# Optimization experiments

Hardware: AMD Instinct MI355X
Metric: run time of the kernel (lower is better)

## Reference

```python
import jax, jax.numpy as jnp
import numpy as np
from functools import partial

CHANNEL_N = 16
FIRE_RATE = 0.5
SCALE_GROWTH = 1.0
SCALE_GROWTH_SYNTH = 1.0
ANGLE = 0.0


def _sobel_kernels(angle, channel_n):
    # dx = outer([1,2,1],[-1,0,1])/8 ; dy = dx.T ; rotated by angle (degrees)
    dx = np.outer([1.0, 2.0, 1.0], [-1.0, 0.0, 1.0]) / 8.0
    dy = dx.T
    c, s = np.cos(angle * np.pi / 180.0), np.sin(angle * np.pi / 180.0)
    w1 = (c * dx - s * dy).astype(np.float32)
    w2 = (s * dx + c * dy).astype(np.float32)
    # depthwise conv weights, OIHW with O=channel_n, I=1 (groups=channel_n)
    k1 = jnp.asarray(np.tile(w1[None, None], (channel_n, 1, 1, 1)))
    k2 = jnp.asarray(np.tile(w2[None, None], (channel_n, 1, 1, 1)))
    return k1, k2


def _depthwise(x_nchw, k):
    return jax.lax.conv_general_dilated(
        x_nchw, k, window_strides=(1, 1), padding=((1, 1), (1, 1)),
        dimension_numbers=('NCHW', 'OIHW', 'NCHW'),
        feature_group_count=x_nchw.shape[1])


def _alive(x_nchw):
    # 3x3 max-pool (stride 1, pad 1) on channel 1, threshold 0.1
    a = x_nchw[:, 1:2]
    m = jax.lax.reduce_window(a, -jnp.inf, jax.lax.max,
                              (1, 1, 3, 3), (1, 1, 1, 1),
                              ((0, 0), (0, 0), (1, 1), (1, 1)))
    return m > 0.1


def _update(x, w0, b0, w1, key):
    # x: [B,H,W,C]; torch does x.transpose(1,3) -> [B,C,W,H]
    xt = jnp.transpose(x, (0, 3, 2, 1))
    pre_life = _alive(xt)
    k1, k2 = _sobel_kernels(ANGLE, xt.shape[1])
    y = jnp.concatenate([xt, _depthwise(xt, k1), _depthwise(xt, k2)], axis=1)  # [B,3C,W,H]
    d = jnp.transpose(y, (0, 3, 2, 1))  # [B,H,W,3C]
    h = jax.nn.relu(jnp.einsum('bhwc,cd->bhwd', d, w0) + b0)
    dx = jnp.einsum('bhwd,dc->bhwc', h, w1)
    stoch = (jax.random.uniform(key, dx.shape[:3] + (1,)) > FIRE_RATE).astype(dx.dtype)
    dx = dx * stoch * (SCALE_GROWTH * SCALE_GROWTH_SYNTH)
    xt = xt + jnp.transpose(dx, (0, 3, 2, 1))
    post_life = _alive(xt)
    xt = xt * (pre_life & post_life).astype(xt.dtype)
    return jnp.transpose(xt, (0, 3, 2, 1))


def setup_inputs() -> dict:
    key = jax.random.key(0)
    k1, k2, k3, k4 = jax.random.split(key, 4)
    B, H, W, C, HID = 16, 256, 256, CHANNEL_N, 128
    x = jax.random.uniform(k1, (B, H, W, C), dtype=jnp.float32)
    w0 = jax.random.normal(k2, (3 * C, HID), dtype=jnp.float32) * 0.05
    b0 = jax.random.normal(k3, (HID,), dtype=jnp.float32) * 0.05
    w1 = jax.random.normal(k4, (HID, C), dtype=jnp.float32) * 0.05
    return {'x': x, 'w0': w0, 'b0': b0, 'w1': w1, 'steps': 1}


def reference(x, w0, b0, w1, steps):
    key = jax.random.key(42)
    for step in range(steps):
        x = _update(x, w0, b0, w1, jax.random.fold_in(key, step))
    return x
```

## Files before the change

### kernel.cpp

```cpp
#include <hip/hip_runtime.h>
#include <hip/hip_bf16.h>

#define BB 16
#define HH 256
#define WW 256
#define CC 16
#define HID 128
#define NPIX (BB*HH*WW)
#define NBLK2 2048

#define PCL_STRIDE 36
#define PCL_WAVE2  (128*PCL_STRIDE)

typedef __attribute__((ext_vector_type(8))) short s16x8;
typedef __attribute__((ext_vector_type(4))) float f32x4;

union V8 { uint4 u; uint2 h[2]; s16x8 s; };

struct Key2 { unsigned a, b; };

__host__ __device__ constexpr unsigned rotl32c(unsigned x, int d) {
    return (x << d) | (x >> (32 - d));
}

__host__ __device__ constexpr Key2 tf2x32(unsigned k0, unsigned k1, unsigned x0, unsigned x1) {
    const unsigned ks2 = k0 ^ k1 ^ 0x1BD11BDAu;
    const int R[5][4] = {{13,15,26,6},{17,29,16,24},{13,15,26,6},{17,29,16,24},{13,15,26,6}};
    const unsigned ka[5] = {k1, ks2, k0, k1, ks2};
    const unsigned kb[5] = {ks2, k0, k1, ks2, k0};
    x0 += k0; x1 += k1;
    for (int i = 0; i < 5; ++i) {
        for (int j = 0; j < 4; ++j) { x0 += x1; x1 = rotl32c(x1, R[i][j]); x1 ^= x0; }
        x0 += ka[i]; x1 += kb[i] + (unsigned)(i + 1);
    }
    return Key2{x0, x1};
}
constexpr Key2 FK = tf2x32(0u, 42u, 0u, 0u);

__device__ inline unsigned pk2(float a, float b) {
    union { __hip_bfloat162 h2; unsigned u; } cv;
    cv.h2 = __float22bfloat162_rn(make_float2(a, b));
    return cv.u;
}
__device__ inline float unpk_lo(unsigned u) { return __uint_as_float(u << 16); }
__device__ inline float unpk_hi(unsigned u) { return __uint_as_float(u & 0xffff0000u); }

__global__ __launch_bounds__(256)
void ca_prep(const float* __restrict__ w0, const float* __restrict__ w1,
             short* __restrict__ w0bf, short* __restrict__ w1bf)
{
    const int t = threadIdx.x;
    const int blk = blockIdx.x;
    if (blk < 4) {
        const int row = blk * 256 + t;
        const int l15 = row & 15, g = (row >> 4) & 3, ks = (row >> 6) & 1;
        const int nt = (row >> 7) & 1, p = row >> 8;
        const int n = p * 32 + nt * 16 + l15;
        float v[8];
        #pragma unroll
        for (int jj = 0; jj < 8; ++jj) {
            const int kg = ks * 32 + g * 8 + jj;
            v[jj] = (kg < 48) ? w0[kg * HID + n] : 0.0f;
        }
        uint4 pkv;
        pkv.x = pk2(v[0], v[1]); pkv.y = pk2(v[2], v[3]);
        pkv.z = pk2(v[4], v[5]); pkv.w = pk2(v[6], v[7]);
        *reinterpret_cast<uint4*>(&w0bf[row * 8]) = pkv;
    } else {
        const int l15 = t & 15, g = (t >> 4) & 3, p = t >> 6;
        float v[8];
        #pragma unroll
        for (int e = 0; e < 8; ++e) v[e] = w1[(p * 32 + g * 8 + e) * CC + l15];
        uint4 pkv;
        pkv.x = pk2(v[0], v[1]); pkv.y = pk2(v[2], v[3]);
        pkv.z = pk2(v[4], v[5]); pkv.w = pk2(v[6], v[7]);
        *reinterpret_cast<uint4*>(&w1bf[t * 8]) = pkv;
    }
}

__global__ __launch_bounds__(256, 4)
void ca_fused(const float* __restrict__ x, const short* __restrict__ w0bf,
              const float* __restrict__ b0, const short* __restrict__ w1bf,
              float* __restrict__ out, float* __restrict__ ch1new,
              unsigned char* __restrict__ prelife)
{
    __shared__ short percL[4 * PCL_WAVE2];
    __shared__ unsigned slotLp[4][2][16];
    __shared__ unsigned slotRp[4][2][16];
    __shared__ float    slotLm[4][2];
    __shared__ float    slotRm[4][2];

    const int tid = threadIdx.x;
    const unsigned bid = blockIdx.x;
    const unsigned lb = (bid & 7u) * 256u + (bid >> 3);
    const int hpair = lb & 127;
    const unsigned jbase = lb * 512u;
    const int wave = tid >> 6, lane = tid & 63;
    const int l15 = lane & 15, g = lane >> 4;

    const float* pR1 = x + ((size_t)jbase + tid) * CC;
    float4 R0[4], R1[4], R2[4], R3[4];
    #pragma unroll
    for (int q = 0; q < 4; ++q) R1[q] = *reinterpret_cast<const float4*>(pR1 + q * 4);
    #pragma unroll
    for (int q = 0; q < 4; ++q) R2[q] = *reinterpret_cast<const float4*>(pR1 + WW * CC + q * 4);
    if (hpair > 0) {
        #pragma unroll
        for (int q = 0; q < 4; ++q) R0[q] = *reinterpret_cast<const float4*>(pR1 - WW * CC + q * 4);
    } else {
        #pragma unroll
        for (int q = 0; q < 4; ++q) R0[q] = make_float4(0.f, 0.f, 0.f, 0.f);
    }
    if (hpair < 127) {
        #pragma unroll
        for (int q = 0; q < 4; ++q) R3[q] = *reinterpret_cast<const float4*>(pR1 + 2 * WW * CC + q * 4);
    } else {
        #pragma unroll
        for (int q = 0; q < 4; ++q) R3[q] = make_float4(0.f, 0.f, 0.f, 0.f);
    }

    unsigned pkA[16], pkB[16];
    #pragma unroll
    for (int q = 0; q < 4; ++q) {
        const float4 a = R0[q], bb = R1[q], c = R2[q], d = R3[q];
        const float a_[4] = {a.x, a.y, a.z, a.w};
        const float b_[4] = {bb.x, bb.y, bb.z, bb.w};
        const float c_[4] = {c.x, c.y, c.z, c.w};
        const float d_[4] = {d.x, d.y, d.z, d.w};
        #pragma unroll
        for (int e = 0; e < 4; ++e) {
            const int ch = q * 4 + e;
            pkA[ch] = pk2(c_[e] - a_[e], fmaf(2.f, b_[e], a_[e] + c_[e]));
            pkB[ch] = pk2(d_[e] - b_[e], fmaf(2.f, c_[e], b_[e] + d_[e]));
        }
    }
    const float M1 = fmaxf(fmaxf(R0[0].y, R1[0].y), R2[0].y);
    const float M2 = fmaxf(fmaxf(R1[0].y, R2[0].y), R3[0].y);

    if (lane == 0) {
        #pragma unroll
        for (int c = 0; c < 16; ++c) { slotRp[wave][0][c] = pkA[c]; slotRp[wave][1][c] = pkB[c]; }
        slotRm[wave][0] = M1; slotRm[wave][1] = M2;
    }
    if (lane == 63) {
        #pragma unroll
        for (int c = 0; c < 16; ++c) { slotLp[wave][0][c] = pkA[c]; slotLp[wave][1][c] = pkB[c]; }
        slotLm[wave][0] = M1; slotLm[wave][1] = M2;
    }
    __syncthreads();

    unsigned long long kmask[2];
    float maxc1v[2];
    #pragma unroll
    for (int rs = 0; rs < 2; ++rs) {
        const unsigned* pk = (rs == 0) ? pkA : pkB;
        float conv[32];
        #pragma unroll
        for (int hf = 0; hf < 2; ++hf) {
            const int c0 = hf * 8;
            unsigned pL[8], pR[8];
            #pragma unroll
            for (int c = 0; c < 8; ++c) {
                pL[c] = __shfl_up(pk[c0 + c], 1);
                pR[c] = __shfl_down(pk[c0 + c], 1);
            }
            if (lane == 0) {
                #pragma unroll
                for (int c = 0; c < 8; ++c)
                    pL[c] = (tid == 0) ? 0u : slotLp[wave - 1][rs][c0 + c];
            }
            if (lane == 63) {
                #pragma unroll
                for (int c = 0; c < 8; ++c)
                    pR[c] = (tid == 255) ? 0u : slotRp[wave + 1][rs][c0 + c];
            }
            #pragma unroll
            for (int c = 0; c < 8; ++c) {
                const float Dm = unpk_lo(pk[c0 + c]);
                conv[c0 + c]      = 0.125f * (unpk_lo(pL[c]) + unpk_lo(pR[c]) + 2.f * Dm);
                conv[16 + c0 + c] = 0.125f * (unpk_hi(pR[c]) - unpk_hi(pL[c]));
            }
        }
        const int base = wave * PCL_WAVE2 + (rs * 64 + lane) * PCL_STRIDE;
        #pragma unroll
        for (int c = 0; c < 8; ++c) {
            uint2 pkv;
            pkv.x = pk2(conv[c*4 + 0], conv[c*4 + 1]);
            pkv.y = pk2(conv[c*4 + 2], conv[c*4 + 3]);
            *reinterpret_cast<uint2*>(&percL[base + c * 4]) = pkv;
        }
        const float M = (rs == 0) ? M1 : M2;
        float Ml = __shfl_up(M, 1), Mr = __shfl_down(M, 1);
        if (lane == 0)  Ml = (tid == 0)   ? -3.0e38f : slotLm[wave - 1][rs];
        if (lane == 63) Mr = (tid == 255) ? -3.0e38f : slotRm[wave + 1][rs];
        maxc1v[rs] = fmaxf(fmaxf(Ml, M), Mr);
        const unsigned j = jbase + rs * 256 + tid;
        const Key2 r = tf2x32(FK.a, FK.b, 0u, j);
        const unsigned bits = r.a ^ r.b;
        const float uu = __uint_as_float((bits >> 9) | 0x3f800000u) - 1.0f;
        kmask[rs] = __ballot(uu > 0.5f);
        prelife[j] = (maxc1v[rs] > 0.1f) ? (unsigned char)1 : (unsigned char)0;
    }

    const s16x8* w0F = reinterpret_cast<const s16x8*>(w0bf);
    const s16x8* w1F = reinterpret_cast<const s16x8*>(w1bf);

    #pragma unroll
    for (int rs = 0; rs < 2; ++rs) {
        const unsigned pixbase = jbase + rs * 256 + wave * 64;
        const int halfbase = wave * PCL_WAVE2 + rs * 64 * PCL_STRIDE;

        s16x8 pB0[4], pB1[4];
        #pragma unroll
        for (int mt = 0; mt < 4; ++mt) {
            const int prow = halfbase + (mt * 16 + l15) * PCL_STRIDE;
            V8 f0, f1;
            if (g < 2) {
                const float* xp = &x[(size_t)(pixbase + mt * 16 + l15) * CC + g * 8];
                const float4 va = *reinterpret_cast<const float4*>(xp);
                const float4 vb = *reinterpret_cast<const float4*>(xp + 4);
                f0.u.x = pk2(va.x, va.y); f0.u.y = pk2(va.z, va.w);
                f0.u.z = pk2(vb.x, vb.y); f0.u.w = pk2(vb.z, vb.w);
                f1.h[0] = *reinterpret_cast<const uint2*>(&percL[prow + 16 + g * 8]);
                f1.h[1] = *reinterpret_cast<const uint2*>(&percL[prow + 16 + g * 8 + 4]);
            } else {
                f0.h[0] = *reinterpret_cast<const uint2*>(&percL[prow + (g - 2) * 8]);
                f0.h[1] = *reinterpret_cast<const uint2*>(&percL[prow + (g - 2) * 8 + 4]);
                f1.u = make_uint4(0u, 0u, 0u, 0u);
            }
            pB0[mt] = f0.s;
            pB1[mt] = f1.s;
        }

        __builtin_amdgcn_sched_barrier(0);

        short* HPw = &percL[halfbase];
        f32x4 acc2[4];
        #pragma unroll
        for (int mt2 = 0; mt2 < 4; ++mt2) acc2[mt2] = 0.0f;

        #pragma unroll
        for (int p = 0; p < 4; ++p) {
            s16x8 w0f0[2], w0f1[2];
            #pragma unroll
            for (int nt = 0; nt < 2; ++nt) {
                w0f0[nt] = w0F[((p * 2 + nt) * 2 + 0) * 64 + lane];
                w0f1[nt] = w0F[((p * 2 + nt) * 2 + 1) * 64 + lane];
            }
            #pragma unroll
            for (int mt = 0; mt < 4; ++mt) {
                #pragma unroll
                for (int nt = 0; nt < 2; ++nt) {
                    const float4 bv = *reinterpret_cast<const float4*>(&b0[p*32 + nt*16 + g*4]);
                    f32x4 acc = {bv.x, bv.y, bv.z, bv.w};
                    acc = __builtin_amdgcn_mfma_f32_16x16x32_bf16(w0f0[nt], pB0[mt], acc, 0, 0, 0);
                    acc = __builtin_amdgcn_mfma_f32_16x16x32_bf16(w0f1[nt], pB1[mt], acc, 0, 0, 0);
                    uint2 hv;
                    hv.x = pk2(fmaxf(acc[0], 0.f), fmaxf(acc[1], 0.f));
                    hv.y = pk2(fmaxf(acc[2], 0.f), fmaxf(acc[3], 0.f));
                    const int m = mt * 16 + l15;
                    *reinterpret_cast<uint2*>(
                        &HPw[m * 32 + 4 * ((4*nt + g) ^ (l15 & 6))]) = hv;
                }
            }
            {
                const s16x8 wf = w1F[p * 64 + lane];
                #pragma unroll
                for (int mt2 = 0; mt2 < 4; ++mt2) {
                    const int m = mt2 * 16 + l15;
                    const s16x8 hp = *reinterpret_cast<const s16x8*>(
                        &HPw[m * 32 + 4 * ((2*g) ^ (l15 & 6))]);
                    acc2[mt2] = __builtin_amdgcn_mfma_f32_16x16x32_bf16(wf, hp, acc2[mt2], 0, 0, 0);
                }
            }
        }

        #pragma unroll
        for (int mt2 = 0; mt2 < 4; ++mt2) {
            const int prel = mt2 * 16 + l15;
            const unsigned pj = pixbase + prel;
            const float kv = ((kmask[rs] >> prel) & 1ull) ? 1.0f : 0.0f;
            const float4 x4 = *reinterpret_cast<const float4*>(&x[(size_t)pj * CC + g * 4]);
            float4 v;
            v.x = x4.x + acc2[mt2][0] * kv;
            v.y = x4.y + acc2[mt2][1] * kv;
            v.z = x4.z + acc2[mt2][2] * kv;
            v.w = x4.w + acc2[mt2][3] * kv;
            *reinterpret_cast<float4*>(&out[(size_t)pj * CC + g * 4]) = v;
            if (g == 0) ch1new[pj] = v.y;
        }
    }
}

__global__ __launch_bounds__(256)
void ca_step2(float* __restrict__ out, const float* __restrict__ ch1new,
              const unsigned char* __restrict__ prelife)
{
    const int tid = threadIdx.x;
    const int lane = tid & 63;
    const int rowi = tid >> 6;
    const unsigned bid = blockIdx.x;
    const int hq = bid & 63, b = bid >> 6;
    const int h = hq * 4 + rowi;
    const unsigned rowbase = ((unsigned)(b * HH + h)) * WW;
    const int w0 = lane * 4;

    float4 vc = *reinterpret_cast<const float4*>(&ch1new[rowbase + w0]);
    float m0 = vc.x, m1 = vc.y, m2 = vc.z, m3 = vc.w;
    if (h > 0) {
        float4 vu = *reinterpret_cast<const float4*>(&ch1new[rowbase - WW + w0]);
        m0 = fmaxf(m0, vu.x); m1 = fmaxf(m1, vu.y); m2 = fmaxf(m2, vu.z); m3 = fmaxf(m3, vu.w);
    }
    if (h < HH - 1) {
        float4 vd = *reinterpret_cast<const float4*>(&ch1new[rowbase + WW + w0]);
        m0 = fmaxf(m0, vd.x); m1 = fmaxf(m1, vd.y); m2 = fmaxf(m2, vd.z); m3 = fmaxf(m3, vd.w);
    }
    float left  = __shfl_up(m3, 1);   if (lane == 0)  left  = -3.0e38f;
    float right = __shfl_down(m0, 1); if (lane == 63) right = -3.0e38f;

    float mm[4];
    mm[0] = fmaxf(fmaxf(left, m0), m1);
    mm[1] = fmaxf(fmaxf(m0, m1), m2);
    mm[2] = fmaxf(fmaxf(m1, m2), m3);
    mm[3] = fmaxf(fmaxf(m2, m3), right);

    const uchar4 pl = *reinterpret_cast<const uchar4*>(&prelife[rowbase + w0]);
    const unsigned char pla[4] = {pl.x, pl.y, pl.z, pl.w};
    #pragma unroll
    for (int i = 0; i < 4; ++i) {
        const bool alive = (pla[i] != 0) && (mm[i] > 0.1f);
        if (!alive) {
            const float4 z = make_float4(0.f, 0.f, 0.f, 0.f);
            float4* o = reinterpret_cast<float4*>(out + (size_t)(rowbase + w0 + i) * CC);
            o[0] = z; o[1] = z; o[2] = z; o[3] = z;
        }
    }
}

extern "C" void kernel_launch(void* const* d_in, const int* in_sizes, int n_in,
                              void* d_out, int out_size, void* d_ws, size_t ws_size,
                              hipStream_t stream) {
    const float* x  = (const float*)d_in[0];
    const float* w0 = (const float*)d_in[1];
    const float* b0 = (const float*)d_in[2];
    const float* w1 = (const float*)d_in[3];
    float* out = (float*)d_out;

    float* ch1new = (float*)d_ws;
    unsigned char* prelife = (unsigned char*)d_ws + (size_t)NPIX * 4;
    short* w0bf = (short*)((char*)d_ws + 5242880);
    short* w1bf = (short*)((char*)d_ws + 5242880 + 16384);

    ca_prep<<<dim3(5), dim3(256), 0, stream>>>(w0, w1, w0bf, w1bf);
    ca_fused<<<dim3(NBLK2), dim3(256), 0, stream>>>(x, w0bf, b0, w1bf, out, ch1new, prelife);
    ca_step2<<<dim3(NPIX / 1024), dim3(256), 0, stream>>>(out, ch1new, prelife);
}
```

Before: 69.44 us.

## Process both row-sets together in the MLP loop to share weight fragments

The two row-set halves of each wave's MLP work are merged into one loop over hidden-chunks p. Each w0/w1 fragment and bias load now serves both halves, and each step has twice as many independent MFMA chains. The input fragments for both halves are loaded up front, and the hidden scratch row stride changes from 32 to the percL stride of 36. This roughly doubles the live fragment and accumulator registers, so launch bounds drop from 4 to 3 waves-per-EU, trading occupancy for reuse and ILP.

```diff
diff --git a/kernel.cpp b/kernel.cpp
--- a/kernel.cpp
+++ b/kernel.cpp
@@ -78,7 +78,7 @@
     }
 }
 
-__global__ __launch_bounds__(256, 4)
+__global__ __launch_bounds__(256, 3)
 void ca_fused(const float* __restrict__ x, const short* __restrict__ w0bf,
               const float* __restrict__ b0, const short* __restrict__ w1bf,
               float* __restrict__ out, float* __restrict__ ch1new,
@@ -150,7 +150,6 @@
     __syncthreads();
 
     unsigned long long kmask[2];
-    float maxc1v[2];
     #pragma unroll
     for (int rs = 0; rs < 2; ++rs) {
         const unsigned* pk = (rs == 0) ? pkA : pkB;
@@ -193,24 +192,23 @@
         float Ml = __shfl_up(M, 1), Mr = __shfl_down(M, 1);
         if (lane == 0)  Ml = (tid == 0)   ? -3.0e38f : slotLm[wave - 1][rs];
         if (lane == 63) Mr = (tid == 255) ? -3.0e38f : slotRm[wave + 1][rs];
-        maxc1v[rs] = fmaxf(fmaxf(Ml, M), Mr);
+        const float maxc1 = fmaxf(fmaxf(Ml, M), Mr);
         const unsigned j = jbase + rs * 256 + tid;
         const Key2 r = tf2x32(FK.a, FK.b, 0u, j);
         const unsigned bits = r.a ^ r.b;
         const float uu = __uint_as_float((bits >> 9) | 0x3f800000u) - 1.0f;
         kmask[rs] = __ballot(uu > 0.5f);
-        prelife[j] = (maxc1v[rs] > 0.1f) ? (unsigned char)1 : (unsigned char)0;
+        prelife[j] = (maxc1 > 0.1f) ? (unsigned char)1 : (unsigned char)0;
     }
 
     const s16x8* w0F = reinterpret_cast<const s16x8*>(w0bf);
     const s16x8* w1F = reinterpret_cast<const s16x8*>(w1bf);
 
+    s16x8 pB0[2][4], pB1[2][4];
     #pragma unroll
     for (int rs = 0; rs < 2; ++rs) {
         const unsigned pixbase = jbase + rs * 256 + wave * 64;
         const int halfbase = wave * PCL_WAVE2 + rs * 64 * PCL_STRIDE;
-
-        s16x8 pB0[4], pB1[4];
         #pragma unroll
         for (int mt = 0; mt < 4; ++mt) {
             const int prow = halfbase + (mt * 16 + l15) * PCL_STRIDE;
@@ -228,53 +226,63 @@
                 f0.h[1] = *reinterpret_cast<const uint2*>(&percL[prow + (g - 2) * 8 + 4]);
                 f1.u = make_uint4(0u, 0u, 0u, 0u);
             }
-            pB0[mt] = f0.s;
-            pB1[mt] = f1.s;
-        }
-
-        __builtin_amdgcn_sched_barrier(0);
-
-        short* HPw = &percL[halfbase];
-        f32x4 acc2[4];
-        #pragma unroll
-        for (int mt2 = 0; mt2 < 4; ++mt2) acc2[mt2] = 0.0f;
-
-        #pragma unroll
-        for (int p = 0; p < 4; ++p) {
-            s16x8 w0f0[2], w0f1[2];
+            pB0[rs][mt] = f0.s;
+            pB1[rs][mt] = f1.s;
+        }
+    }
+
+    __builtin_amdgcn_sched_barrier(0);
+
+    f32x4 acc2[2][4];
+    #pragma unroll
+    for (int rs = 0; rs < 2; ++rs)
+        #pragma unroll
+        for (int mt2 = 0; mt2 < 4; ++mt2) acc2[rs][mt2] = 0.0f;
+
+    #pragma unroll
+    for (int p = 0; p < 4; ++p) {
+        s16x8 w0f0[2], w0f1[2];
+        #pragma unroll
+        for (int nt = 0; nt < 2; ++nt) {
+            w0f0[nt] = w0F[((p * 2 + nt) * 2 + 0) * 64 + lane];
+            w0f1[nt] = w0F[((p * 2 + nt) * 2 + 1) * 64 + lane];
+        }
+        const s16x8 wf = w1F[p * 64 + lane];
+
+        #pragma unroll
+        for (int mt = 0; mt < 4; ++mt) {
             #pragma unroll
             for (int nt = 0; nt < 2; ++nt) {
-                w0f0[nt] = w0F[((p * 2 + nt) * 2 + 0) * 64 + lane];
-                w0f1[nt] = w0F[((p * 2 + nt) * 2 + 1) * 64 + lane];
-            }
-            #pragma unroll
-            for (int mt = 0; mt < 4; ++mt) {
+                const float4 bv = *reinterpret_cast<const float4*>(&b0[p*32 + nt*16 + g*4]);
                 #pragma unroll
-                for (int nt = 0; nt < 2; ++nt) {
-                    const float4 bv = *reinterpret_cast<const float4*>(&b0[p*32 + nt*16 + g*4]);
+                for (int rs = 0; rs < 2; ++rs) {
                     f32x4 acc = {bv.x, bv.y, bv.z, bv.w};
-                    acc = __builtin_amdgcn_mfma_f32_16x16x32_bf16(w0f0[nt], pB0[mt], acc, 0, 0, 0);
-                    acc = __builtin_amdgcn_mfma_f32_16x16x32_bf16(w0f1[nt], pB1[mt], acc, 0, 0, 0);
+                    acc = __builtin_amdgcn_mfma_f32_16x16x32_bf16(w0f0[nt], pB0[rs][mt], acc, 0, 0, 0);
+                    acc = __builtin_amdgcn_mfma_f32_16x16x32_bf16(w0f1[nt], pB1[rs][mt], acc, 0, 0, 0);
                     uint2 hv;
                     hv.x = pk2(fmaxf(acc[0], 0.f), fmaxf(acc[1], 0.f));
                     hv.y = pk2(fmaxf(acc[2], 0.f), fmaxf(acc[3], 0.f));
-                    const int m = mt * 16 + l15;
+                    short* HPw = &percL[wave * PCL_WAVE2 + rs * 64 * PCL_STRIDE];
                     *reinterpret_cast<uint2*>(
-                        &HPw[m * 32 + 4 * ((4*nt + g) ^ (l15 & 6))]) = hv;
+                        &HPw[(mt * 16 + l15) * PCL_STRIDE + 4 * ((4*nt + g) ^ (l15 & 6))]) = hv;
                 }
             }
-            {
-                const s16x8 wf = w1F[p * 64 + lane];
-                #pragma unroll
-                for (int mt2 = 0; mt2 < 4; ++mt2) {
-                    const int m = mt2 * 16 + l15;
-                    const s16x8 hp = *reinterpret_cast<const s16x8*>(
-                        &HPw[m * 32 + 4 * ((2*g) ^ (l15 & 6))]);
-                    acc2[mt2] = __builtin_amdgcn_mfma_f32_16x16x32_bf16(wf, hp, acc2[mt2], 0, 0, 0);
-                }
-            }
-        }
-
+        }
+        #pragma unroll
+        for (int rs = 0; rs < 2; ++rs) {
+            short* HPw = &percL[wave * PCL_WAVE2 + rs * 64 * PCL_STRIDE];
+            #pragma unroll
+            for (int mt2 = 0; mt2 < 4; ++mt2) {
+                const s16x8 hp = *reinterpret_cast<const s16x8*>(
+                    &HPw[(mt2 * 16 + l15) * PCL_STRIDE + 4 * ((2*g) ^ (l15 & 6))]);
+                acc2[rs][mt2] = __builtin_amdgcn_mfma_f32_16x16x32_bf16(wf, hp, acc2[rs][mt2], 0, 0, 0);
+            }
+        }
+    }
+
+    #pragma unroll
+    for (int rs = 0; rs < 2; ++rs) {
+        const unsigned pixbase = jbase + rs * 256 + wave * 64;
         #pragma unroll
         for (int mt2 = 0; mt2 < 4; ++mt2) {
             const int prel = mt2 * 16 + l15;
@@ -282,10 +290,10 @@
             const float kv = ((kmask[rs] >> prel) & 1ull) ? 1.0f : 0.0f;
             const float4 x4 = *reinterpret_cast<const float4*>(&x[(size_t)pj * CC + g * 4]);
             float4 v;
-            v.x = x4.x + acc2[mt2][0] * kv;
-            v.y = x4.y + acc2[mt2][1] * kv;
-            v.z = x4.z + acc2[mt2][2] * kv;
-            v.w = x4.w + acc2[mt2][3] * kv;
+            v.x = x4.x + acc2[rs][mt2][0] * kv;
+            v.y = x4.y + acc2[rs][mt2][1] * kv;
+            v.z = x4.z + acc2[rs][mt2][2] * kv;
+            v.w = x4.w + acc2[rs][mt2][3] * kv;
             *reinterpret_cast<float4*>(&out[(size_t)pj * CC + g * 4]) = v;
             if (g == 0) ch1new[pj] = v.y;
         }
```

Result: slower. 87.24 us (+25.6%).
